# Kernel tuning notes

Hardware: AMD Instinct MI355X
Metric: run time of the kernel (lower is better)

## Reference

```python
import jax, jax.numpy as jnp
import numpy as np

B, T, D_MODEL, H, RPR_K = 2, 2048, 1024, 16, 8
DK = D_MODEL // H  # 64
NUM_RPR = 2 * RPR_K + 1


def setup_inputs() -> dict:
    key = jax.random.key(0)
    ks = jax.random.split(key, 16)
    s = 0.02
    inp = {
        "query": jax.random.normal(ks[0], (B, T, D_MODEL), jnp.float32),
        "key": jax.random.normal(ks[1], (B, T, D_MODEL), jnp.float32),
        "value": jax.random.normal(ks[2], (B, T, D_MODEL), jnp.float32),
        "mask": jnp.ones((B, 1, 1, T), dtype=bool),
        "w_q": jax.random.normal(ks[3], (D_MODEL, H * DK), jnp.float32) * s,
        "b_q": jnp.zeros((H * DK,), jnp.float32),
        "w_k": jax.random.normal(ks[4], (D_MODEL, H * DK), jnp.float32) * s,
        "b_k": jnp.zeros((H * DK,), jnp.float32),
        "w_v": jax.random.normal(ks[5], (D_MODEL, H * DK), jnp.float32) * s,
        "b_v": jnp.zeros((H * DK,), jnp.float32),
        "w_o": jax.random.normal(ks[6], (H * DK, D_MODEL), jnp.float32) * s,
        "b_o": jnp.zeros((D_MODEL,), jnp.float32),
        "rpr_key_table": jax.random.normal(ks[7], (NUM_RPR, DK), jnp.float32),
        "rpr_value_table": jax.random.normal(ks[8], (NUM_RPR, DK), jnp.float32),
    }
    return inp


def _rel_edges(seq_len):
    # edges[i, j] = clamp(j - i + rpr_k, 0, 2*rpr_k)  -> [T, T] int32
    seq = jnp.arange(seq_len)
    edges = seq[None, :] - seq[:, None] + RPR_K
    return jnp.clip(edges, 0, 2 * RPR_K)


def reference(query, key, value, mask, w_q, b_q, w_k, b_k, w_v, b_v,
              w_o, b_o, rpr_key_table, rpr_value_table):
    Bsz, Tlen, _ = query.shape
    edges = _rel_edges(Tlen)                       # [T, T]
    ek = rpr_key_table[edges]                      # [T, T, DK]
    ev = rpr_value_table[edges]                    # [T, T, DK]

    def proj(x, w, b):
        return (x @ w + b).reshape(Bsz, Tlen, H, DK).transpose(0, 2, 1, 3)  # [B,H,T,DK]

    q = proj(query, w_q, b_q)
    k = proj(key, w_k, b_k)
    v = proj(value, w_v, b_v)

    scores_qk = jnp.einsum('bhtd,bhsd->bhts', q, k)
    scores_qek = jnp.einsum('bhtd,tsd->bhts', q, ek)
    scores = (scores_qk + scores_qek) / jnp.sqrt(jnp.float32(DK))
    scores = jnp.where(mask, scores, jnp.float32(-1e9))
    a = jax.nn.softmax(scores, axis=-1)            # [B,H,T,T]

    upd = jnp.einsum('bhts,bhsd->bhtd', a, v)
    upd_e = jnp.einsum('bhts,tsd->bhtd', a, ev)
    x = (upd + upd_e).transpose(0, 2, 1, 3).reshape(Bsz, Tlen, H * DK)
    return x @ w_o + b_o
```

## Files before the change

kernel.cpp:

```cpp
#include <hip/hip_runtime.h>
#include <stdint.h>


typedef unsigned short u16;
typedef __attribute__((ext_vector_type(4))) float f32x4;
typedef __attribute__((ext_vector_type(16))) float f32x16;
typedef __attribute__((ext_vector_type(4))) int   i32x4;
typedef __attribute__((ext_vector_type(8))) __bf16 bh8;

#define T_LEN 2048
#define NHEAD 16
#define NR    17

#define SCALE_LOG2 0.18033688011112042f
#define CLAMP_LOG2 86.56170245333781f

__device__ __forceinline__ float bf2f(u16 x) {
  unsigned u = ((unsigned)x) << 16;
  return __builtin_bit_cast(float, u);
}
__device__ __forceinline__ u16 f2bf(float f) {
  unsigned u = __builtin_bit_cast(unsigned, f);
  u = u + 0x7fffu + ((u >> 16) & 1u);
  return (u16)(u >> 16);
}
__device__ __forceinline__ f32x4 zero4() { f32x4 z = {0.f, 0.f, 0.f, 0.f}; return z; }
__device__ __forceinline__ f32x16 zero16() {
  f32x16 z = {0.f, 0.f, 0.f, 0.f, 0.f, 0.f, 0.f, 0.f,
              0.f, 0.f, 0.f, 0.f, 0.f, 0.f, 0.f, 0.f};
  return z;
}

__device__ __forceinline__ f32x4 mfma16(bh8 a, bh8 b, f32x4 c) {
  return __builtin_amdgcn_mfma_f32_16x16x32_bf16(a, b, c, 0, 0, 0);
}
__device__ __forceinline__ f32x16 mfma32(bh8 a, bh8 b, f32x16 c) {
  return __builtin_amdgcn_mfma_f32_32x32x16_bf16(a, b, c, 0, 0, 0);
}

__device__ __forceinline__ unsigned cvtpk(float a, float b) {
  unsigned r;
  asm("v_cvt_pk_bf16_f32 %0, %1, %2" : "=v"(r) : "v"(a), "v"(b));
  return r;
}

__device__ __forceinline__ void bar_sync() {
  __builtin_amdgcn_sched_barrier(0);
  asm volatile("s_waitcnt lgkmcnt(0)" ::: "memory");
  __builtin_amdgcn_s_barrier();
  __builtin_amdgcn_sched_barrier(0);
}

__device__ __forceinline__ void wait_vm0() {
  __builtin_amdgcn_sched_barrier(0);
  asm volatile("s_waitcnt vmcnt(0)" ::: "memory");
  __builtin_amdgcn_sched_barrier(0);
}

__device__ __forceinline__ void async16(const u16* g, u16* l) {
  __builtin_amdgcn_global_load_lds(
      (const __attribute__((address_space(1))) void*)g,
      (__attribute__((address_space(3))) void*)l, 16, 0, 0);
}

__device__ __forceinline__ bh8 ldfrag(const u16* base, int row, int qc) {
  const i32x4 v = *(const i32x4*)(base + row * 64 + ((qc ^ (row & 7)) << 3));
  return __builtin_bit_cast(bh8, v);
}

__global__ __launch_bounds__(256) void prep_kernel(
    const float* __restrict__ xq, const float* __restrict__ xk,
    const float* __restrict__ xv, const float* __restrict__ w0,
    const float* __restrict__ w1, const float* __restrict__ w2,
    const float* __restrict__ w3, u16* __restrict__ oq, u16* __restrict__ ok,
    u16* __restrict__ ov, u16* __restrict__ t0, u16* __restrict__ t1,
    u16* __restrict__ t2, u16* __restrict__ t3) {
  __shared__ u16 tile[32][33];
  const int z = blockIdx.z;
  if (z < 3) {
    const float* S = (z == 0) ? xq : (z == 1) ? xk : xv;
    u16* D = (z == 0) ? oq : (z == 1) ? ok : ov;
    const size_t i = ((size_t)blockIdx.x * 256 + threadIdx.x) * 8;
    const f32x4 v0 = *(const f32x4*)(S + i);
    const f32x4 v1 = *(const f32x4*)(S + i + 4);
    u16 o[8];
#pragma unroll
    for (int j = 0; j < 4; ++j) {
      o[j] = f2bf(v0[j]);
      o[4 + j] = f2bf(v1[j]);
    }
    i32x4 w;
    __builtin_memcpy(&w, o, 16);
    *(i32x4*)(D + i) = w;
  } else {
    if (blockIdx.x >= 1024) return;
    const float* S = (z == 3) ? w0 : (z == 4) ? w1 : (z == 5) ? w2 : w3;
    u16* D = (z == 3) ? t0 : (z == 4) ? t1 : (z == 5) ? t2 : t3;
    const int tx = threadIdx.x & 31, ty = threadIdx.x >> 5;
    const int bx = blockIdx.x & 31, by = blockIdx.x >> 5;
#pragma unroll
    for (int i = 0; i < 4; ++i) {
      const int y = by * 32 + ty + i * 8;
      tile[ty + i * 8][tx] = f2bf(S[(size_t)y * 1024 + bx * 32 + tx]);
    }
    __syncthreads();
#pragma unroll
    for (int i = 0; i < 4; ++i) {
      const int y = bx * 32 + ty + i * 8;
      D[(size_t)y * 1024 + by * 32 + tx] = tile[tx][ty + i * 8];
    }
  }
}

__device__ __forceinline__ void gemm_body(const u16* __restrict__ A,
                                          const u16* __restrict__ Bm,
                                          const float* __restrict__ bias,
                                          void* __restrict__ out, int mode,
                                          int bm, int bn) {
  __shared__ __align__(16) u16 As[2][128 * 32];
  __shared__ __align__(16) u16 Bs[2][128 * 32];
  const int tid = threadIdx.x;
  const int wv = tid >> 6;
  const int ln = tid & 63;
  const int quad = ln >> 4, l15 = ln & 15;
  const int wr = wv >> 1, wc = wv & 1;

  f32x4 acc[4][4];
#pragma unroll
  for (int i = 0; i < 4; ++i)
#pragma unroll
    for (int j = 0; j < 4; ++j) acc[i][j] = zero4();

  const int c0 = tid, c1 = tid + 256;
  const size_t aoff0 = (size_t)(bm * 128 + (c0 >> 2)) * 1024 + (c0 & 3) * 8;
  const size_t aoff1 = (size_t)(bm * 128 + (c1 >> 2)) * 1024 + (c1 & 3) * 8;
  const size_t boff0 = (size_t)(bn * 128 + (c0 >> 2)) * 1024 + (c0 & 3) * 8;
  const size_t boff1 = (size_t)(bn * 128 + (c1 >> 2)) * 1024 + (c1 & 3) * 8;

  u16* ad0[2] = {&As[0][(wv * 64) * 8], &As[1][(wv * 64) * 8]};
  u16* ad1[2] = {&As[0][(256 + wv * 64) * 8], &As[1][(256 + wv * 64) * 8]};
  u16* bd0[2] = {&Bs[0][(wv * 64) * 8], &Bs[1][(wv * 64) * 8]};
  u16* bd1[2] = {&Bs[0][(256 + wv * 64) * 8], &Bs[1][(256 + wv * 64) * 8]};

  async16(A + aoff0, ad0[0]);
  async16(A + aoff1, ad1[0]);
  async16(Bm + boff0, bd0[0]);
  async16(Bm + boff1, bd1[0]);
  __syncthreads();

  for (int kt = 0; kt < 32; ++kt) {
    const int cur = kt & 1, nxt = cur ^ 1;
    if (kt < 31) {
      const int ko = (kt + 1) * 32;
      async16(A + aoff0 + ko, ad0[nxt]);
      async16(A + aoff1 + ko, ad1[nxt]);
      async16(Bm + boff0 + ko, bd0[nxt]);
      async16(Bm + boff1 + ko, bd1[nxt]);
    }

    bh8 af[4], bf[4];
#pragma unroll
    for (int mi = 0; mi < 4; ++mi)
      af[mi] = __builtin_bit_cast(
          bh8,
          *(const i32x4*)&As[cur][(wr * 64 + mi * 16 + l15) * 32 + quad * 8]);
#pragma unroll
    for (int ni = 0; ni < 4; ++ni)
      bf[ni] = __builtin_bit_cast(
          bh8,
          *(const i32x4*)&Bs[cur][(wc * 64 + ni * 16 + l15) * 32 + quad * 8]);
#pragma unroll
    for (int mi = 0; mi < 4; ++mi)
#pragma unroll
      for (int ni = 0; ni < 4; ++ni)
        acc[mi][ni] = mfma16(af[mi], bf[ni], acc[mi][ni]);

    __syncthreads();
  }

#pragma unroll
  for (int mi = 0; mi < 4; ++mi) {
    const int row0 = bm * 128 + wr * 64 + mi * 16 + quad * 4;
#pragma unroll
    for (int ni = 0; ni < 4; ++ni) {
      const int col = bn * 128 + wc * 64 + ni * 16 + l15;
      const float bcol = (mode == 3) ? 0.f : bias[col];
#pragma unroll
      for (int reg = 0; reg < 4; ++reg) {
        const int r = row0 + reg;
        const float v = acc[mi][ni][reg] + ((mode == 3) ? bias[r] : bcol);
        if (mode == 0) {
          ((float*)out)[(size_t)r * 1024 + col] = v;
        } else if (mode == 1) {
          const int bb = r >> 11, t = r & 2047;
          const int h = col >> 6, d = col & 63;
          ((u16*)out)[(((size_t)bb * NHEAD + h) * T_LEN + (size_t)t) * 64 + d] =
              f2bf(v);
        } else {
          const int h = r >> 6, d = r & 63;
          const int bb = col >> 11, t = col & 2047;
          ((u16*)out)[(((size_t)bb * NHEAD + h) * 64 + (size_t)d) * T_LEN + t] =
              f2bf(v);
        }
      }
    }
  }
}

__global__ __launch_bounds__(256) void gemm_qkv_kernel(
    const u16* __restrict__ xq, const u16* __restrict__ xk,
    const u16* __restrict__ xv, const u16* __restrict__ wtq,
    const u16* __restrict__ wtk, const u16* __restrict__ wtv,
    const float* __restrict__ bq, const float* __restrict__ bk,
    const float* __restrict__ bv, u16* __restrict__ oq, u16* __restrict__ ok,
    u16* __restrict__ ovt) {
  const int z = blockIdx.z;
  if (z == 0)
    gemm_body(xq, wtq, bq, oq, 1, blockIdx.x, blockIdx.y);
  else if (z == 1)
    gemm_body(xk, wtk, bk, ok, 1, blockIdx.x, blockIdx.y);
  else
    gemm_body(wtv, xv, bv, ovt, 3, blockIdx.y, blockIdx.x);
}

__global__ __launch_bounds__(256) void gemm_o_kernel(const u16* __restrict__ X,
                                                     const u16* __restrict__ Wt,
                                                     const float* __restrict__ bias,
                                                     float* __restrict__ out) {
  gemm_body(X, Wt, bias, out, 0, blockIdx.x, blockIdx.y);
}

__global__ __launch_bounds__(256) void attn_kernel(
    const u16* __restrict__ Qw, const u16* __restrict__ Kw,
    const u16* __restrict__ Vtw, const float* __restrict__ rkt,
    const float* __restrict__ rvt, u16* __restrict__ U) {
  __shared__ __align__(16) u16 smu[24576];
  __shared__ float smf[5568];
  u16* const Qs = smu;
  float* const qes = smf;
  float* const aw = smf + 2176;
  float* const lp = smf + 4352;
  float* const rvs = smf + 4480;

  const int tid = threadIdx.x;
  const int wv = tid >> 6, ln = tid & 63;
  const int l31 = ln & 31, hi = ln >> 5;
  const int wg = blockIdx.x;
  const int xcd = wg & 7;
  const int slot = wg >> 3;
  const int qt = slot & 15;
  const int bh = xcd * 4 + (slot >> 4);
  const size_t hb = (size_t)bh * (T_LEN * 64);
  const int t0 = qt * 128 + wv * 32;
  const int tl = wv * 32 + l31;

  const int r8 = ln >> 3, c8 = ln & 7;
  const int kgp = c8 ^ (r8 & 7);
  const u16* ksrc0 = Kw + hb + (size_t)(wv * 16 + r8) * 64 + kgp * 8;
  const u16* ksrc1 = Kw + hb + (size_t)(wv * 16 + 8 + r8) * 64 + kgp * 8;
  const u16* vsrc0 = Vtw + hb + (size_t)(wv * 16 + r8) * T_LEN + kgp * 8;
  const u16* vsrc1 = Vtw + hb + (size_t)(wv * 16 + 8 + r8) * T_LEN + kgp * 8;
  u16* const ldsK0 = smu + 8192 + (wv * 16) * 64;
  u16* const ldsK1 = smu + 8192 + (wv * 16 + 8) * 64;
  u16* const ldsV0 = smu + 16384 + (wv * 16) * 64;
  u16* const ldsV1 = smu + 16384 + (wv * 16 + 8) * 64;

  {
    const u16* qsrc = Qw + hb + (size_t)(qt * 128 + wv * 32 + r8) * 64 + kgp * 8;
#pragma unroll
    for (int a = 0; a < 4; ++a)
      async16(qsrc + (size_t)(a * 8) * 64, Qs + (wv * 32 + a * 8) * 64);
  }
  async16(ksrc0, ldsK0);
  async16(ksrc1, ldsK1);
  async16(vsrc0, ldsV0);
  async16(vsrc1, ldsV1);
  wait_vm0();
  bar_sync();

  for (int i = tid; i < 128 * NR; i += 256) {
    const int row = i / NR, r = i - row * NR;
    float s = 0.f;
#pragma unroll
    for (int c = 0; c < 8; ++c) {
      const i32x4 qv = *(const i32x4*)&Qs[row * 64 + ((c ^ (row & 7)) << 3)];
      const u16* qq = (const u16*)&qv;
#pragma unroll
      for (int j = 0; j < 8; ++j) s += bf2f(qq[j]) * rkt[r * 64 + c * 8 + j];
    }
    qes[i] = s;
    aw[i] = 0.f;
  }
  bar_sync();

  const float qb0 = qes[tl * NR + 0] * SCALE_LOG2;
  const float qb16 = qes[tl * NR + 16] * SCALE_LOG2;
  bh8 qf[4];
#pragma unroll
  for (int kb = 0; kb < 4; ++kb) qf[kb] = ldfrag(Qs, tl, kb * 2 + hi);

  float l_l = 0.f, s0_l = 0.f, s16_l = 0.f;
  f32x16 oacc[2] = {zero16(), zero16()};

  for (int st = 0; st < 32; ++st) {
    const int cur = st & 1;
    const u16* Kc = smu + 8192 + cur * 4096;
    const u16* Vc = smu + 16384 + cur * 4096;
    if (st < 31) {
      const int nxt = cur ^ 1;
      async16(ksrc0 + (size_t)(st + 1) * 4096, ldsK0 + nxt * 4096);
      async16(ksrc1 + (size_t)(st + 1) * 4096, ldsK1 + nxt * 4096);
      async16(vsrc0 + (size_t)(st + 1) * 64, ldsV0 + nxt * 4096);
      async16(vsrc1 + (size_t)(st + 1) * 64, ldsV1 + nxt * 4096);
    }
    __builtin_amdgcn_s_setprio(1);

#pragma unroll
    for (int sb = 0; sb < 2; ++sb) {
      f32x16 sacc = zero16();
#pragma unroll
      for (int kb = 0; kb < 4; ++kb) {
        const bh8 kf = ldfrag(Kc, sb * 32 + l31, kb * 2 + hi);
        sacc = mfma32(kf, qf[kb], sacc);
      }

      const int sbase = st * 64 + sb * 32;
      float p[16];
      if (sbase + 39 <= t0) {
        float ts = 0.f;
#pragma unroll
        for (int r = 0; r < 16; ++r) {
          const float x = fminf(sacc[r] * SCALE_LOG2 + qb0, CLAMP_LOG2);
          const float pv = __builtin_amdgcn_exp2f(x);
          p[r] = pv;
          ts += pv;
        }
        l_l += ts;
        s0_l += ts;
      } else if (sbase >= t0 + 39) {
        float ts = 0.f;
#pragma unroll
        for (int r = 0; r < 16; ++r) {
          const float x = fminf(sacc[r] * SCALE_LOG2 + qb16, CLAMP_LOG2);
          const float pv = __builtin_amdgcn_exp2f(x);
          p[r] = pv;
          ts += pv;
        }
        l_l += ts;
        s16_l += ts;
      } else {
        const int base = sbase + 4 * hi - (t0 + l31) + 8;
#pragma unroll
        for (int r = 0; r < 16; ++r) {
          int rel = base + (r & 3) + 8 * (r >> 2);
          rel = rel < 0 ? 0 : (rel > 16 ? 16 : rel);
          const float x = fminf((sacc[r] + qes[tl * NR + rel]) * SCALE_LOG2,
                                CLAMP_LOG2);
          const float pv = __builtin_amdgcn_exp2f(x);
          p[r] = pv;
          l_l += pv;
          if (rel == 0)
            s0_l += pv;
          else if (rel == 16)
            s16_l += pv;
          else
            atomicAdd(&aw[tl * NR + rel], pv);
        }
      }

#pragma unroll
      for (int h = 0; h < 2; ++h) {
        unsigned wa = cvtpk(p[8 * h + 0], p[8 * h + 1]);
        unsigned wb = cvtpk(p[8 * h + 2], p[8 * h + 3]);
        unsigned wc = cvtpk(p[8 * h + 4], p[8 * h + 5]);
        unsigned wd = cvtpk(p[8 * h + 6], p[8 * h + 7]);
        asm("v_permlane32_swap_b32 %0, %1" : "+v"(wa), "+v"(wc));
        asm("v_permlane32_swap_b32 %0, %1" : "+v"(wb), "+v"(wd));
        const i32x4 fr = {(int)wa, (int)wb, (int)wc, (int)wd};
        const bh8 pa = __builtin_bit_cast(bh8, fr);
        const int ks = sb * 2 + h;
#pragma unroll
        for (int db = 0; db < 2; ++db) {
          const bh8 vf = ldfrag(Vc, db * 32 + l31, ks * 2 + hi);
          oacc[db] = mfma32(pa, vf, oacc[db]);
        }
      }
    }
    __builtin_amdgcn_s_setprio(0);

    wait_vm0();
    bar_sync();
  }

  l_l += __shfl_xor(l_l, 32);
  s0_l += __shfl_xor(s0_l, 32);
  s16_l += __shfl_xor(s16_l, 32);
  if (ln < 32) lp[tl] = l_l;
  for (int i = tid; i < NR * 64; i += 256) rvs[i] = rvt[i];
  __syncthreads();
  if (ln < 32) {
    aw[tl * NR + 0] += s0_l;
    aw[tl * NR + 16] += s16_l;
  }
  __syncthreads();

  const int bb = bh >> 4, hh = bh & 15;
#pragma unroll
  for (int r = 0; r < 16; ++r) {
    const int srow = (r & 3) + 8 * (r >> 2) + 4 * hi;
    const int trow = wv * 32 + srow;
    const float linv = 1.f / lp[trow];
    float e0 = 0.f, e1 = 0.f;
#pragma unroll
    for (int rr = 0; rr < NR; ++rr) {
      const float awv = aw[trow * NR + rr];
      e0 += awv * rvs[rr * 64 + l31];
      e1 += awv * rvs[rr * 64 + 32 + l31];
    }
    const int tg = qt * 128 + trow;
    const size_t ubase = ((size_t)bb * T_LEN + tg) * 1024 + hh * 64;
    U[ubase + l31] = f2bf((oacc[0][r] + e0) * linv);
    U[ubase + 32 + l31] = f2bf((oacc[1][r] + e1) * linv);
  }
}

extern "C" void kernel_launch(void* const* d_in, const int* in_sizes, int n_in,
                              void* d_out, int out_size, void* d_ws,
                              size_t ws_size, hipStream_t stream) {
  const float* query = (const float*)d_in[0];
  const float* key = (const float*)d_in[1];
  const float* value = (const float*)d_in[2];
  const float* w_q = (const float*)d_in[4];
  const float* b_q = (const float*)d_in[5];
  const float* w_k = (const float*)d_in[6];
  const float* b_k = (const float*)d_in[7];
  const float* w_v = (const float*)d_in[8];
  const float* b_v = (const float*)d_in[9];
  const float* w_o = (const float*)d_in[10];
  const float* b_o = (const float*)d_in[11];
  const float* rkt = (const float*)d_in[12];
  const float* rvt = (const float*)d_in[13];

  char* ws = (char*)d_ws;
  const size_t MB2 = 1u << 21, MB8 = 1u << 23;
  u16* wtq = (u16*)(ws + 0 * MB2);
  u16* wtk = (u16*)(ws + 1 * MB2);
  u16* wtv = (u16*)(ws + 2 * MB2);
  u16* wto = (u16*)(ws + 3 * MB2);
  u16* Xq = (u16*)(ws + 4 * MB2 + 0 * MB8);
  u16* Xk = (u16*)(ws + 4 * MB2 + 1 * MB8);
  u16* Xv = (u16*)(ws + 4 * MB2 + 2 * MB8);
  u16* Qw = (u16*)(ws + 4 * MB2 + 3 * MB8);
  u16* Kw = (u16*)(ws + 4 * MB2 + 4 * MB8);
  u16* Vtw = (u16*)(ws + 4 * MB2 + 5 * MB8);
  u16* Uw = (u16*)(ws + 4 * MB2 + 6 * MB8);

  prep_kernel<<<dim3(2048, 1, 7), 256, 0, stream>>>(
      query, key, value, w_q, w_k, w_v, w_o, Xq, Xk, Xv, wtq, wtk, wtv, wto);
  gemm_qkv_kernel<<<dim3(32, 8, 3), 256, 0, stream>>>(
      Xq, Xk, Xv, wtq, wtk, wtv, b_q, b_k, b_v, Qw, Kw, Vtw);
  attn_kernel<<<dim3(512), 256, 0, stream>>>(Qw, Kw, Vtw, rkt, rvt, Uw);
  gemm_o_kernel<<<dim3(32, 8), 256, 0, stream>>>(Uw, wto, b_o, (float*)d_out);
}
```

Baseline: 283.1 us.

## Shrink attention LDS footprint for 3 blocks/CU and retile output GEMM

The attention kernel now aliases the Q tile region with the K/V double buffers by loading Q and computing the q·rk table before fetching K/V. The dense aw array shrinks to 15 middle buckets plus separate edge arrays, and the rvs table reuses the freed smu space. Together these cut LDS use enough that launch_bounds can request 3 blocks per CU. The output projection gets its own 64x128 tile GEMM with double-buffered async loads, doubling the grid to 512 blocks so more CUs are busy. The cost is an extra barrier and serialized K/V prefetch at attention start, plus possible register pressure from the occupancy bound.

```diff
diff --git a/kernel.cpp b/kernel.cpp
--- a/kernel.cpp
+++ b/kernel.cpp
@@ -189,9 +189,7 @@
       for (int reg = 0; reg < 4; ++reg) {
         const int r = row0 + reg;
         const float v = acc[mi][ni][reg] + ((mode == 3) ? bias[r] : bcol);
-        if (mode == 0) {
-          ((float*)out)[(size_t)r * 1024 + col] = v;
-        } else if (mode == 1) {
+        if (mode == 1) {
           const int bb = r >> 11, t = r & 2047;
           const int h = col >> 6, d = col & 63;
           ((u16*)out)[(((size_t)bb * NHEAD + h) * T_LEN + (size_t)t) * 64 + d] =
@@ -223,24 +221,95 @@
     gemm_body(wtv, xv, bv, ovt, 3, blockIdx.y, blockIdx.x);
 }
 
-__global__ __launch_bounds__(256) void gemm_o_kernel(const u16* __restrict__ X,
-                                                     const u16* __restrict__ Wt,
+__global__ __launch_bounds__(256) void gemm_o_kernel(const u16* __restrict__ A,
+                                                     const u16* __restrict__ Bm,
                                                      const float* __restrict__ bias,
                                                      float* __restrict__ out) {
-  gemm_body(X, Wt, bias, out, 0, blockIdx.x, blockIdx.y);
-}
-
-__global__ __launch_bounds__(256) void attn_kernel(
+  __shared__ __align__(16) u16 As[2][64 * 32];
+  __shared__ __align__(16) u16 Bs[2][128 * 32];
+  const int tid = threadIdx.x;
+  const int wv = tid >> 6;
+  const int ln = tid & 63;
+  const int quad = ln >> 4, l15 = ln & 15;
+  const int wr = wv >> 1, wc = wv & 1;
+  const int bm = blockIdx.x, bn = blockIdx.y;
+
+  f32x4 acc[2][4];
+#pragma unroll
+  for (int i = 0; i < 2; ++i)
+#pragma unroll
+    for (int j = 0; j < 4; ++j) acc[i][j] = zero4();
+
+  const int c0 = tid, c1 = tid + 256;
+  const size_t aoff0 = (size_t)(bm * 64 + (c0 >> 2)) * 1024 + (c0 & 3) * 8;
+  const size_t boff0 = (size_t)(bn * 128 + (c0 >> 2)) * 1024 + (c0 & 3) * 8;
+  const size_t boff1 = (size_t)(bn * 128 + (c1 >> 2)) * 1024 + (c1 & 3) * 8;
+
+  u16* ad0[2] = {&As[0][(wv * 64) * 8], &As[1][(wv * 64) * 8]};
+  u16* bd0[2] = {&Bs[0][(wv * 64) * 8], &Bs[1][(wv * 64) * 8]};
+  u16* bd1[2] = {&Bs[0][(256 + wv * 64) * 8], &Bs[1][(256 + wv * 64) * 8]};
+
+  async16(A + aoff0, ad0[0]);
+  async16(Bm + boff0, bd0[0]);
+  async16(Bm + boff1, bd1[0]);
+  __syncthreads();
+
+  for (int kt = 0; kt < 32; ++kt) {
+    const int cur = kt & 1, nxt = cur ^ 1;
+    if (kt < 31) {
+      const int ko = (kt + 1) * 32;
+      async16(A + aoff0 + ko, ad0[nxt]);
+      async16(Bm + boff0 + ko, bd0[nxt]);
+      async16(Bm + boff1 + ko, bd1[nxt]);
+    }
+
+    bh8 af[2], bf[4];
+#pragma unroll
+    for (int mi = 0; mi < 2; ++mi)
+      af[mi] = __builtin_bit_cast(
+          bh8,
+          *(const i32x4*)&As[cur][(wr * 32 + mi * 16 + l15) * 32 + quad * 8]);
+#pragma unroll
+    for (int ni = 0; ni < 4; ++ni)
+      bf[ni] = __builtin_bit_cast(
+          bh8,
+          *(const i32x4*)&Bs[cur][(wc * 64 + ni * 16 + l15) * 32 + quad * 8]);
+#pragma unroll
+    for (int mi = 0; mi < 2; ++mi)
+#pragma unroll
+      for (int ni = 0; ni < 4; ++ni)
+        acc[mi][ni] = mfma16(af[mi], bf[ni], acc[mi][ni]);
+
+    __syncthreads();
+  }
+
+#pragma unroll
+  for (int mi = 0; mi < 2; ++mi) {
+    const int row0 = bm * 64 + wr * 32 + mi * 16 + quad * 4;
+#pragma unroll
+    for (int ni = 0; ni < 4; ++ni) {
+      const int col = bn * 128 + wc * 64 + ni * 16 + l15;
+      const float bcol = bias[col];
+#pragma unroll
+      for (int reg = 0; reg < 4; ++reg)
+        out[(size_t)(row0 + reg) * 1024 + col] = acc[mi][ni][reg] + bcol;
+    }
+  }
+}
+
+__global__ __launch_bounds__(256, 3) void attn_kernel(
     const u16* __restrict__ Qw, const u16* __restrict__ Kw,
     const u16* __restrict__ Vtw, const float* __restrict__ rkt,
     const float* __restrict__ rvt, u16* __restrict__ U) {
-  __shared__ __align__(16) u16 smu[24576];
-  __shared__ float smf[5568];
+  __shared__ __align__(16) u16 smu[16384];
+  __shared__ float smf[4480];
   u16* const Qs = smu;
   float* const qes = smf;
-  float* const aw = smf + 2176;
-  float* const lp = smf + 4352;
-  float* const rvs = smf + 4480;
+  float* const aw15 = smf + 2176;
+  float* const lp = smf + 4096;
+  float* const aw0 = smf + 4224;
+  float* const aw16 = smf + 4352;
+  float* const rvs = (float*)smu;
 
   const int tid = threadIdx.x;
   const int wv = tid >> 6, ln = tid & 63;
@@ -260,10 +329,10 @@
   const u16* ksrc1 = Kw + hb + (size_t)(wv * 16 + 8 + r8) * 64 + kgp * 8;
   const u16* vsrc0 = Vtw + hb + (size_t)(wv * 16 + r8) * T_LEN + kgp * 8;
   const u16* vsrc1 = Vtw + hb + (size_t)(wv * 16 + 8 + r8) * T_LEN + kgp * 8;
-  u16* const ldsK0 = smu + 8192 + (wv * 16) * 64;
-  u16* const ldsK1 = smu + 8192 + (wv * 16 + 8) * 64;
-  u16* const ldsV0 = smu + 16384 + (wv * 16) * 64;
-  u16* const ldsV1 = smu + 16384 + (wv * 16 + 8) * 64;
+  u16* const ldsK0 = smu + (wv * 16) * 64;
+  u16* const ldsK1 = smu + (wv * 16 + 8) * 64;
+  u16* const ldsV0 = smu + 8192 + (wv * 16) * 64;
+  u16* const ldsV1 = smu + 8192 + (wv * 16 + 8) * 64;
 
   {
     const u16* qsrc = Qw + hb + (size_t)(qt * 128 + wv * 32 + r8) * 64 + kgp * 8;
@@ -271,6 +340,31 @@
     for (int a = 0; a < 4; ++a)
       async16(qsrc + (size_t)(a * 8) * 64, Qs + (wv * 32 + a * 8) * 64);
   }
+  wait_vm0();
+  bar_sync();
+
+  for (int i = tid; i < 128 * NR; i += 256) {
+    const int row = i / NR, r = i - row * NR;
+    float s = 0.f;
+#pragma unroll
+    for (int c = 0; c < 8; ++c) {
+      const i32x4 qv = *(const i32x4*)&Qs[row * 64 + ((c ^ (row & 7)) << 3)];
+      const u16* qq = (const u16*)&qv;
+#pragma unroll
+      for (int j = 0; j < 8; ++j) s += bf2f(qq[j]) * rkt[r * 64 + c * 8 + j];
+    }
+    qes[i] = s;
+  }
+  for (int i = tid; i < 128 * 15; i += 256) aw15[i] = 0.f;
+  bar_sync();
+
+  const float qb0 = qes[tl * NR + 0] * SCALE_LOG2;
+  const float qb16 = qes[tl * NR + 16] * SCALE_LOG2;
+  bh8 qf[4];
+#pragma unroll
+  for (int kb = 0; kb < 4; ++kb) qf[kb] = ldfrag(Qs, tl, kb * 2 + hi);
+  bar_sync();
+
   async16(ksrc0, ldsK0);
   async16(ksrc1, ldsK1);
   async16(vsrc0, ldsV0);
@@ -278,34 +372,13 @@
   wait_vm0();
   bar_sync();
 
-  for (int i = tid; i < 128 * NR; i += 256) {
-    const int row = i / NR, r = i - row * NR;
-    float s = 0.f;
-#pragma unroll
-    for (int c = 0; c < 8; ++c) {
-      const i32x4 qv = *(const i32x4*)&Qs[row * 64 + ((c ^ (row & 7)) << 3)];
-      const u16* qq = (const u16*)&qv;
-#pragma unroll
-      for (int j = 0; j < 8; ++j) s += bf2f(qq[j]) * rkt[r * 64 + c * 8 + j];
-    }
-    qes[i] = s;
-    aw[i] = 0.f;
-  }
-  bar_sync();
-
-  const float qb0 = qes[tl * NR + 0] * SCALE_LOG2;
-  const float qb16 = qes[tl * NR + 16] * SCALE_LOG2;
-  bh8 qf[4];
-#pragma unroll
-  for (int kb = 0; kb < 4; ++kb) qf[kb] = ldfrag(Qs, tl, kb * 2 + hi);
-
   float l_l = 0.f, s0_l = 0.f, s16_l = 0.f;
   f32x16 oacc[2] = {zero16(), zero16()};
 
   for (int st = 0; st < 32; ++st) {
     const int cur = st & 1;
-    const u16* Kc = smu + 8192 + cur * 4096;
-    const u16* Vc = smu + 16384 + cur * 4096;
+    const u16* Kc = smu + cur * 4096;
+    const u16* Vc = smu + 8192 + cur * 4096;
     if (st < 31) {
       const int nxt = cur ^ 1;
       async16(ksrc0 + (size_t)(st + 1) * 4096, ldsK0 + nxt * 4096);
@@ -364,7 +437,7 @@
           else if (rel == 16)
             s16_l += pv;
           else
-            atomicAdd(&aw[tl * NR + rel], pv);
+            atomicAdd(&aw15[tl * 15 + rel - 1], pv);
         }
       }
 
@@ -395,13 +468,12 @@
   l_l += __shfl_xor(l_l, 32);
   s0_l += __shfl_xor(s0_l, 32);
   s16_l += __shfl_xor(s16_l, 32);
-  if (ln < 32) lp[tl] = l_l;
+  if (ln < 32) {
+    lp[tl] = l_l;
+    aw0[tl] = s0_l;
+    aw16[tl] = s16_l;
+  }
   for (int i = tid; i < NR * 64; i += 256) rvs[i] = rvt[i];
-  __syncthreads();
-  if (ln < 32) {
-    aw[tl * NR + 0] += s0_l;
-    aw[tl * NR + 16] += s16_l;
-  }
   __syncthreads();
 
   const int bb = bh >> 4, hh = bh & 15;
@@ -410,10 +482,11 @@
     const int srow = (r & 3) + 8 * (r >> 2) + 4 * hi;
     const int trow = wv * 32 + srow;
     const float linv = 1.f / lp[trow];
-    float e0 = 0.f, e1 = 0.f;
-#pragma unroll
-    for (int rr = 0; rr < NR; ++rr) {
-      const float awv = aw[trow * NR + rr];
+    float e0 = aw0[trow] * rvs[l31] + aw16[trow] * rvs[16 * 64 + l31];
+    float e1 = aw0[trow] * rvs[32 + l31] + aw16[trow] * rvs[16 * 64 + 32 + l31];
+#pragma unroll
+    for (int rr = 1; rr < 16; ++rr) {
+      const float awv = aw15[trow * 15 + rr - 1];
       e0 += awv * rvs[rr * 64 + l31];
       e1 += awv * rvs[rr * 64 + 32 + l31];
     }
@@ -460,5 +533,5 @@
   gemm_qkv_kernel<<<dim3(32, 8, 3), 256, 0, stream>>>(
       Xq, Xk, Xv, wtq, wtk, wtv, b_q, b_k, b_v, Qw, Kw, Vtw);
   attn_kernel<<<dim3(512), 256, 0, stream>>>(Qw, Kw, Vtw, rkt, rvt, Uw);
-  gemm_o_kernel<<<dim3(32, 8), 256, 0, stream>>>(Uw, wto, b_o, (float*)d_out);
-}
+  gemm_o_kernel<<<dim3(64, 8), 256, 0, stream>>>(Uw, wto, b_o, (float*)d_out);
+}
```

Result: faster. 271.1 us (-4.3%).
